# Performance work log

Hardware: AMD Instinct MI355X
Metric: run time of the kernel (lower is better)

The kernel has to match this reference:

```python
import jax, jax.numpy as jnp
import numpy as np

# ---- static configuration (mirrors init_kwargs) ----
C_IN = 1
SEQ_LEN = 512
N_KERNELS = 10000
KSS = [7, 9, 11]
KS_MAX = max(KSS)
BATCH = 8


def _make_params(seed=42):
    """Replicates the random kernel generation in RocketFeaturesPytorch.__init__."""
    rng = np.random.RandomState(seed)
    ks = np.empty(N_KERNELS, np.int32)
    dil = np.empty(N_KERNELS, np.int32)
    pad = np.empty(N_KERNELS, np.int32)  # per-side padding actually applied (= 2*padding)
    W = np.zeros((N_KERNELS, C_IN, KS_MAX), np.float32)  # zero-padded to KS_MAX taps
    b = np.empty(N_KERNELS, np.float32)
    for i in range(N_KERNELS):
        k = int(rng.choice(KSS))
        d_f = 2.0 ** rng.uniform(0, np.log2((SEQ_LEN - 1) // (k - 1)))
        d = int(d_f)  # Conv1d dilation uses int(dilation)
        p = int((k - 1) * d_f // 2) if rng.randint(2) == 1 else 0  # padding uses FLOAT dilation (as in source)
        w = rng.randn(1, C_IN, k).astype(np.float32)
        w -= w.mean()
        W[i, :, :k] = w[0]
        b[i] = np.float32(2.0 * (rng.rand() - 0.5))
        ks[i], dil[i], pad[i] = k, d, 2 * p  # layer padding = 2*padding per side
    lo = SEQ_LEN + 2 * pad - dil * (ks - 1)  # per-kernel output length (>=1 guaranteed)
    return W, b, ks, dil, pad, lo

_W, _B, _KS, _DIL, _PAD, _LO = _make_params()
PAD_MAX = int(_PAD.max())
T_MAX = int(_LO.max())


def setup_inputs() -> dict:
    key = jax.random.key(0)
    x = jax.random.normal(key, (BATCH, C_IN, SEQ_LEN), dtype=jnp.float32)
    return {
        "x": x,
        "weights": jnp.asarray(_W),                     # [K, C, KS_MAX]
        "biases": jnp.asarray(_B),                      # [K]
        "base": jnp.asarray(PAD_MAX - _PAD, jnp.int32), # [K] start offset into padded x
        "dil": jnp.asarray(_DIL, jnp.int32),            # [K]
        "lo": jnp.asarray(_LO, jnp.int32),              # [K] valid output length
    }


def reference(x, weights, biases, base, dil, lo):
    B, C, L = x.shape
    K = weights.shape[0]
    xpad = jnp.pad(x, ((0, 0), (0, 0), (PAD_MAX, PAD_MAX)))  # [B, C, Lp]
    Lp = xpad.shape[-1]
    t = jnp.arange(T_MAX, dtype=jnp.int32)                   # [T]

    # dilated conv for all kernels at once: out[b,k,t] = sum_{c,j} w[k,c,j] * xpad[b,c, base[k]+t+j*dil[k]]
    acc = jnp.zeros((B, K, T_MAX), x.dtype)
    for j in range(KS_MAX):  # small static loop over taps
        idx = jnp.clip(base[:, None] + t[None, :] + j * dil[:, None], 0, Lp - 1)  # [K, T]
        g = xpad[:, :, idx]                                   # [B, C, K, T]
        acc = acc + jnp.einsum('bckt,kc->bkt', g, weights[:, :, j])
    out = acc + biases[None, :, None]                         # [B, K, T]

    valid = t[None, :] < lo[:, None]                          # [K, T]
    maxs = jnp.max(jnp.where(valid[None], out, -jnp.inf), axis=-1)                       # [B, K]
    ppv = jnp.sum(jnp.where(valid[None], out > 0, False), axis=-1) / lo[None, :].astype(x.dtype)  # [B, K]

    # original interleaves (max_i, ppv_i) per kernel along the feature dim
    return jnp.stack([maxs, ppv.astype(x.dtype)], axis=-1).reshape(B, 2 * K)
```

## Files before the change

kernel.cpp:

```cpp
#include <hip/hip_runtime.h>
#include <math.h>

#define NK        10000
#define LSEQ      512
#define KSMAX     11
#define NKEY      3072
#define TOT_SLOT  10400
#define GRID_MAIN 1300
#define ROWS_DW   (514 * 4)
#define RED_OFF   ROWS_DW
#define SM_DW     (ROWS_DW + 256 * 10)

typedef _Float16 half2v __attribute__((ext_vector_type(2)));
union H2U { half2v h; unsigned int u; };

__device__ __forceinline__ int ks_index(float w7, float w8, float w9, float w10) {
    if (w7 == 0.f && w8 == 0.f && w9 == 0.f && w10 == 0.f) return 0;
    if (w9 == 0.f && w10 == 0.f) return 1;
    return 2;
}

__global__ __launch_bounds__(1024) void bucket_kernel(
    const float* __restrict__ W, const int* __restrict__ dil, const int* __restrict__ lo,
    int* __restrict__ ord) {
    __shared__ unsigned cnt[NKEY];
    __shared__ unsigned cur[NKEY];
    __shared__ unsigned tot;
    const int tid = threadIdx.x;
    if (tid == 0) tot = 0;
    for (int i = tid; i < NKEY; i += 1024) cnt[i] = 0;
    for (int i = tid; i < TOT_SLOT; i += 1024) ord[i] = -1;
    __syncthreads();
    for (int i = tid; i < NK; i += 1024) {
        const float* wr = W + (size_t)i * KSMAX;
        int ksi = ks_index(wr[7], wr[8], wr[9], wr[10]);
        int d = dil[i];
        int pd = (lo[i] - LSEQ + d * (6 + 2 * ksi)) > 0;
        atomicAdd(&cnt[(((d - 1) * 3 + ksi) << 1) | pd], 1u);
    }
    __syncthreads();
    for (int i = tid; i < NKEY; i += 1024) {
        unsigned c = cnt[i];
        if (c) cur[i] = atomicAdd(&tot, (c + 1u) & ~1u);
    }
    __syncthreads();
    for (int i = tid; i < NK; i += 1024) {
        const float* wr = W + (size_t)i * KSMAX;
        int ksi = ks_index(wr[7], wr[8], wr[9], wr[10]);
        int d = dil[i];
        int pd = (lo[i] - LSEQ + d * (6 + 2 * ksi)) > 0;
        unsigned s = atomicAdd(&cur[(((d - 1) * 3 + ksi) << 1) | pd], 1u);
        ord[s] = i;
    }
}

template <int KS>
__device__ __forceinline__ void run_pair(const float4* __restrict__ rows,
                                         const half2v (&wh)[2][KSMAX], const half2v (&bb)[2],
                                         const int (&pq)[2], const int (&lkq)[2],
                                         int dl, int r_lo, int r_hi, int lane,
                                         half2v (&m)[2][4], half2v (&c)[2][4]) {
    const half2v one2  = {(_Float16)1.0f, (_Float16)1.0f};
    const half2v zero2 = {(_Float16)0.0f, (_Float16)0.0f};
    const half2v big2  = {(_Float16)16384.0f, (_Float16)16384.0f};
    const half2v ninf2 = {(_Float16)(-INFINITY), (_Float16)(-INFINITY)};
    for (int r0 = r_lo; r0 < r_hi; r0 += 64) {
        const int r = r0 + lane;
        half2v a[2][4];
        #pragma unroll
        for (int q = 0; q < 2; ++q) {
            #pragma unroll
            for (int i = 0; i < 4; ++i) a[q][i] = bb[q];
        }
        int pos = r;
        #pragma unroll
        for (int j = 0; j < KS; ++j) {
            int pc = min(max(pos, -1), LSEQ);
            float4 rr = rows[pc + 1];
            half2v v0 = ((half2v*)&rr)[0];
            half2v v1 = ((half2v*)&rr)[1];
            half2v v2 = ((half2v*)&rr)[2];
            half2v v3 = ((half2v*)&rr)[3];
            #pragma unroll
            for (int q = 0; q < 2; ++q) {
                half2v wj = wh[q][j];
                a[q][0] += wj * v0;
                a[q][1] += wj * v1;
                a[q][2] += wj * v2;
                a[q][3] += wj * v3;
            }
            pos += dl;
        }
        #pragma unroll
        for (int q = 0; q < 2; ++q) {
            unsigned t = (unsigned)(r + pq[q]);
            bool valid = t < (unsigned)lkq[q];
            #pragma unroll
            for (int i = 0; i < 4; ++i) {
                half2v av = valid ? a[q][i] : ninf2;
                m[q][i] = __builtin_elementwise_max(m[q][i], av);
                c[q][i] += __builtin_elementwise_min(
                               __builtin_elementwise_max(av * big2, zero2), one2);
            }
        }
    }
}

__global__ __launch_bounds__(256) void rocket_kernel(
    const float* __restrict__ x, const float* __restrict__ W,
    const float* __restrict__ bias, const int* __restrict__ dil,
    const int* __restrict__ lo, const int* __restrict__ ord,
    float* __restrict__ out) {
    __shared__ __align__(16) float sm[SM_DW];
    const int tid = threadIdx.x;
    if (ord[blockIdx.x * 8] < 0) return;

    #pragma unroll
    for (int i = 0; i < 2; ++i) {
        int p = tid + i * 256;
        half2v h0 = {(_Float16)x[0 * LSEQ + p], (_Float16)x[1 * LSEQ + p]};
        half2v h1 = {(_Float16)x[2 * LSEQ + p], (_Float16)x[3 * LSEQ + p]};
        half2v h2 = {(_Float16)x[4 * LSEQ + p], (_Float16)x[5 * LSEQ + p]};
        half2v h3 = {(_Float16)x[6 * LSEQ + p], (_Float16)x[7 * LSEQ + p]};
        float4 v;
        ((half2v*)&v)[0] = h0;
        ((half2v*)&v)[1] = h1;
        ((half2v*)&v)[2] = h2;
        ((half2v*)&v)[3] = h3;
        *(float4*)(sm + (size_t)(p + 1) * 4) = v;
    }
    if (tid < 4)           sm[tid] = 0.0f;
    else if (tid < 8)      sm[513 * 4 + (tid - 4)] = 0.0f;

    const int wave = tid >> 6;
    const int lane = tid & 63;

    int kq[2];
    #pragma unroll
    for (int q = 0; q < 2; ++q)
        kq[q] = __builtin_amdgcn_readfirstlane(ord[blockIdx.x * 8 + wave * 2 + q]);

    half2v wh[2][KSMAX];
    half2v bb[2];
    int pq[2], lkq[2];
    float w7 = 0.f, w8 = 0.f, w9 = 0.f, w10 = 0.f;
    int dl = 1;
    #pragma unroll
    for (int q = 0; q < 2; ++q) {
        int k = kq[q];
        if (k >= 0) {
            const float* wr = W + (size_t)k * KSMAX;
            #pragma unroll
            for (int j = 0; j < KSMAX; ++j) {
                _Float16 wf = (_Float16)wr[j];
                wh[q][j] = (half2v){wf, wf};
            }
            _Float16 bf = (_Float16)bias[k];
            bb[q] = (half2v){bf, bf};
            lkq[q] = lo[k];
            if (q == 0) { w7 = wr[7]; w8 = wr[8]; w9 = wr[9]; w10 = wr[10]; dl = dil[k]; }
        } else {
            #pragma unroll
            for (int j = 0; j < KSMAX; ++j) wh[q][j] = (half2v){(_Float16)0.f, (_Float16)0.f};
            bb[q] = (half2v){(_Float16)0.f, (_Float16)0.f};
            lkq[q] = 0;
        }
    }
    const int ksi = ks_index(w7, w8, w9, w10);
    const int ks = 7 + 2 * ksi;
    int r_lo = 0, r_hi = 0;
    #pragma unroll
    for (int q = 0; q < 2; ++q) {
        if (kq[q] >= 0) {
            pq[q] = (lkq[q] - LSEQ + dl * (ks - 1)) >> 1;
            r_lo = min(r_lo, -pq[q]);
            r_hi = max(r_hi, lkq[q] - pq[q]);
        } else {
            pq[q] = 0;
        }
    }

    __syncthreads();

    const half2v ninf2 = {(_Float16)(-INFINITY), (_Float16)(-INFINITY)};
    const half2v zz    = {(_Float16)0.f, (_Float16)0.f};
    half2v m[2][4], c[2][4];
    #pragma unroll
    for (int q = 0; q < 2; ++q) {
        #pragma unroll
        for (int i = 0; i < 4; ++i) { m[q][i] = ninf2; c[q][i] = zz; }
    }

    const float4* rows = (const float4*)sm;
    if (ksi == 0)      run_pair<7 >(rows, wh, bb, pq, lkq, dl, r_lo, r_hi, lane, m, c);
    else if (ksi == 1) run_pair<9 >(rows, wh, bb, pq, lkq, dl, r_lo, r_hi, lane, m, c);
    else               run_pair<11>(rows, wh, bb, pq, lkq, dl, r_lo, r_hi, lane, m, c);

    unsigned int* red = (unsigned int*)(sm + RED_OFF);
    const int tb = tid * 10;
    const int wbase = (tid & ~63) * 10;
    const int sub = lane & 7;
    const int dv = lane >> 3;
    const bool ismax = dv < 4;
    #pragma unroll
    for (int q = 0; q < 2; ++q) {
        if (kq[q] < 0) continue;
        H2U u0, u1, u2, u3;
        uint2 p01, p23;
        u0.h = m[q][0]; u1.h = m[q][1]; u2.h = m[q][2]; u3.h = m[q][3];
        p01.x = u0.u; p01.y = u1.u; p23.x = u2.u; p23.y = u3.u;
        *(uint2*)(red + tb + 0) = p01;
        *(uint2*)(red + tb + 2) = p23;
        u0.h = c[q][0]; u1.h = c[q][1]; u2.h = c[q][2]; u3.h = c[q][3];
        p01.x = u0.u; p01.y = u1.u; p23.x = u2.u; p23.y = u3.u;
        *(uint2*)(red + tb + 4) = p01;
        *(uint2*)(red + tb + 6) = p23;

        half2v r2 = ismax ? ninf2 : zz;
        #pragma unroll
        for (int i = 0; i < 8; ++i) {
            H2U t;
            t.u = red[wbase + (sub + 8 * i) * 10 + dv];
            r2 = ismax ? __builtin_elementwise_max(r2, t.h) : (r2 + t.h);
        }
        #pragma unroll
        for (int s = 1; s < 8; s <<= 1) {
            H2U me, ot;
            me.h = r2;
            ot.u = (unsigned int)__shfl_xor((int)me.u, s, 64);
            r2 = ismax ? __builtin_elementwise_max(r2, ot.h) : (r2 + ot.h);
        }
        if (sub == 0) {
            int kk = kq[q];
            if (ismax) {
                int b = 2 * dv;
                out[(size_t)b       * (2 * NK) + 2 * kk] = (float)r2.x;
                out[(size_t)(b + 1) * (2 * NK) + 2 * kk] = (float)r2.y;
            } else {
                int b = 2 * (dv - 4);
                float inv = 1.0f / (float)lkq[q];
                out[(size_t)b       * (2 * NK) + 2 * kk + 1] = (float)r2.x * inv;
                out[(size_t)(b + 1) * (2 * NK) + 2 * kk + 1] = (float)r2.y * inv;
            }
        }
    }
}

extern "C" void kernel_launch(void* const* d_in, const int* in_sizes, int n_in,
                              void* d_out, int out_size, void* d_ws, size_t ws_size,
                              hipStream_t stream) {
    const float* x    = (const float*)d_in[0];
    const float* W    = (const float*)d_in[1];
    const float* bias = (const float*)d_in[2];
    const int*   dil  = (const int*)d_in[4];
    const int*   lo   = (const int*)d_in[5];
    float* out = (float*)d_out;
    int* ord = (int*)d_ws;

    bucket_kernel<<<1, 1024, 0, stream>>>(W, dil, lo, ord);
    rocket_kernel<<<GRID_MAIN, 256, 0, stream>>>(x, W, bias, dil, lo, ord, out);
}
```

Measured before the change: 103.6 us.

## Fuse bucketing into main kernel using persistent grid with software grid barriers

Drops the single-block bucket kernel and folds the key counting, prefix scan and slot scatter into the main kernel, separated by two global atomic spin barriers over a fixed grid of 1024 blocks. The main work becomes a grid-stride loop over kernel pairs, and a memset clears the counters beforehand. This removes a serial one-block launch and its dependency gap, but adds global atomics, spin-wait barriers that assume all 1024 blocks are co-resident, and an extra memset call.

```diff
diff --git a/kernel.cpp b/kernel.cpp
--- a/kernel.cpp
+++ b/kernel.cpp
@@ -4,55 +4,25 @@
 #define NK        10000
 #define LSEQ      512
 #define KSMAX     11
-#define NKEY      3072
-#define TOT_SLOT  10400
-#define GRID_MAIN 1300
+#define GRID      1024
+#define NKEYS     512
+#define TOT_SLOT  10512
+
+#define WS_ARR1   0
+#define WS_ARR2   64
+#define WS_CNT    128
+#define WS_OFF    640
+#define WS_ORD    1152
+#define WS_ZERO_BYTES (WS_ORD * 4)
+
 #define ROWS_DW   (514 * 4)
 #define RED_OFF   ROWS_DW
-#define SM_DW     (ROWS_DW + 256 * 10)
+#define SBASE_OFF (ROWS_DW + 2560)
+#define STOT_OFF  (SBASE_OFF + NKEYS)
+#define SM_DW     (STOT_OFF + 1)
 
 typedef _Float16 half2v __attribute__((ext_vector_type(2)));
 union H2U { half2v h; unsigned int u; };
-
-__device__ __forceinline__ int ks_index(float w7, float w8, float w9, float w10) {
-    if (w7 == 0.f && w8 == 0.f && w9 == 0.f && w10 == 0.f) return 0;
-    if (w9 == 0.f && w10 == 0.f) return 1;
-    return 2;
-}
-
-__global__ __launch_bounds__(1024) void bucket_kernel(
-    const float* __restrict__ W, const int* __restrict__ dil, const int* __restrict__ lo,
-    int* __restrict__ ord) {
-    __shared__ unsigned cnt[NKEY];
-    __shared__ unsigned cur[NKEY];
-    __shared__ unsigned tot;
-    const int tid = threadIdx.x;
-    if (tid == 0) tot = 0;
-    for (int i = tid; i < NKEY; i += 1024) cnt[i] = 0;
-    for (int i = tid; i < TOT_SLOT; i += 1024) ord[i] = -1;
-    __syncthreads();
-    for (int i = tid; i < NK; i += 1024) {
-        const float* wr = W + (size_t)i * KSMAX;
-        int ksi = ks_index(wr[7], wr[8], wr[9], wr[10]);
-        int d = dil[i];
-        int pd = (lo[i] - LSEQ + d * (6 + 2 * ksi)) > 0;
-        atomicAdd(&cnt[(((d - 1) * 3 + ksi) << 1) | pd], 1u);
-    }
-    __syncthreads();
-    for (int i = tid; i < NKEY; i += 1024) {
-        unsigned c = cnt[i];
-        if (c) cur[i] = atomicAdd(&tot, (c + 1u) & ~1u);
-    }
-    __syncthreads();
-    for (int i = tid; i < NK; i += 1024) {
-        const float* wr = W + (size_t)i * KSMAX;
-        int ksi = ks_index(wr[7], wr[8], wr[9], wr[10]);
-        int d = dil[i];
-        int pd = (lo[i] - LSEQ + d * (6 + 2 * ksi)) > 0;
-        unsigned s = atomicAdd(&cur[(((d - 1) * 3 + ksi) << 1) | pd], 1u);
-        ord[s] = i;
-    }
-}
 
 template <int KS>
 __device__ __forceinline__ void run_pair(const float4* __restrict__ rows,
@@ -106,14 +76,30 @@
     }
 }
 
-__global__ __launch_bounds__(256) void rocket_kernel(
+__global__ __launch_bounds__(256, 4) void rocket_kernel(
     const float* __restrict__ x, const float* __restrict__ W,
     const float* __restrict__ bias, const int* __restrict__ dil,
-    const int* __restrict__ lo, const int* __restrict__ ord,
+    const int* __restrict__ lo, int* __restrict__ wsI,
     float* __restrict__ out) {
     __shared__ __align__(16) float sm[SM_DW];
-    const int tid = threadIdx.x;
-    if (ord[blockIdx.x * 8] < 0) return;
+    int* smi = (int*)sm;
+    const int tid  = threadIdx.x;
+    const int wave = tid >> 6;
+    const int lane = tid & 63;
+    const int g    = blockIdx.x * 256 + tid;
+
+    int mykey = -1;
+    if (g < NK) {
+        const float* wr = W + (size_t)g * KSMAX;
+        float w7 = wr[7], w8 = wr[8], w9 = wr[9], w10 = wr[10];
+        int ksi = (w7 == 0.f && w8 == 0.f && w9 == 0.f && w10 == 0.f) ? 0
+                : ((w9 == 0.f && w10 == 0.f) ? 1 : 2);
+        int d = dil[g];
+        int pd = (lo[g] - LSEQ + d * (6 + 2 * ksi)) > 0;
+        mykey = (((d - 1) * 3 + ksi) << 1) | pd;
+        atomicAdd(&wsI[WS_CNT + mykey], 1);
+    }
+    if (g < TOT_SLOT) wsI[WS_ORD + g] = -1;
 
     #pragma unroll
     for (int i = 0; i < 2; ++i) {
@@ -132,115 +118,159 @@
     if (tid < 4)           sm[tid] = 0.0f;
     else if (tid < 8)      sm[513 * 4 + (tid - 4)] = 0.0f;
 
-    const int wave = tid >> 6;
-    const int lane = tid & 63;
-
-    int kq[2];
-    #pragma unroll
-    for (int q = 0; q < 2; ++q)
-        kq[q] = __builtin_amdgcn_readfirstlane(ord[blockIdx.x * 8 + wave * 2 + q]);
-
-    half2v wh[2][KSMAX];
-    half2v bb[2];
-    int pq[2], lkq[2];
-    float w7 = 0.f, w8 = 0.f, w9 = 0.f, w10 = 0.f;
-    int dl = 1;
-    #pragma unroll
-    for (int q = 0; q < 2; ++q) {
-        int k = kq[q];
-        if (k >= 0) {
-            const float* wr = W + (size_t)k * KSMAX;
-            #pragma unroll
-            for (int j = 0; j < KSMAX; ++j) {
-                _Float16 wf = (_Float16)wr[j];
-                wh[q][j] = (half2v){wf, wf};
-            }
-            _Float16 bf = (_Float16)bias[k];
-            bb[q] = (half2v){bf, bf};
-            lkq[q] = lo[k];
-            if (q == 0) { w7 = wr[7]; w8 = wr[8]; w9 = wr[9]; w10 = wr[10]; dl = dil[k]; }
-        } else {
-            #pragma unroll
-            for (int j = 0; j < KSMAX; ++j) wh[q][j] = (half2v){(_Float16)0.f, (_Float16)0.f};
-            bb[q] = (half2v){(_Float16)0.f, (_Float16)0.f};
-            lkq[q] = 0;
-        }
-    }
-    const int ksi = ks_index(w7, w8, w9, w10);
-    const int ks = 7 + 2 * ksi;
-    int r_lo = 0, r_hi = 0;
-    #pragma unroll
-    for (int q = 0; q < 2; ++q) {
-        if (kq[q] >= 0) {
-            pq[q] = (lkq[q] - LSEQ + dl * (ks - 1)) >> 1;
-            r_lo = min(r_lo, -pq[q]);
-            r_hi = max(r_hi, lkq[q] - pq[q]);
-        } else {
-            pq[q] = 0;
-        }
-    }
-
-    __syncthreads();
-
-    const half2v ninf2 = {(_Float16)(-INFINITY), (_Float16)(-INFINITY)};
-    const half2v zz    = {(_Float16)0.f, (_Float16)0.f};
-    half2v m[2][4], c[2][4];
-    #pragma unroll
-    for (int q = 0; q < 2; ++q) {
-        #pragma unroll
-        for (int i = 0; i < 4; ++i) { m[q][i] = ninf2; c[q][i] = zz; }
-    }
-
+    __threadfence();
+    __syncthreads();
+    if (tid == 0) {
+        atomicAdd(&wsI[WS_ARR1], 1);
+        while (atomicAdd(&wsI[WS_ARR1], 0) < GRID) {}
+    }
+    __syncthreads();
+
+    if (tid < 64) {
+        unsigned pref[8];
+        unsigned s = 0;
+        #pragma unroll
+        for (int i = 0; i < 8; ++i) {
+            unsigned cc = (unsigned)wsI[WS_CNT + tid * 8 + i];
+            cc = (cc + 1u) & ~1u;
+            pref[i] = s;
+            s += cc;
+        }
+        unsigned sc = s;
+        #pragma unroll
+        for (int o = 1; o < 64; o <<= 1) {
+            unsigned up = (unsigned)__shfl_up((int)sc, o, 64);
+            if (tid >= o) sc += up;
+        }
+        unsigned lanebase = sc - s;
+        #pragma unroll
+        for (int i = 0; i < 8; ++i) smi[SBASE_OFF + tid * 8 + i] = (int)(lanebase + pref[i]);
+        if (tid == 63) smi[STOT_OFF] = (int)sc;
+    }
+    __syncthreads();
+
+    if (g < NK) {
+        int slot = smi[SBASE_OFF + mykey] + atomicAdd(&wsI[WS_OFF + mykey], 1);
+        wsI[WS_ORD + slot] = g;
+    }
+
+    __threadfence();
+    __syncthreads();
+    if (tid == 0) {
+        atomicAdd(&wsI[WS_ARR2], 1);
+        while (atomicAdd(&wsI[WS_ARR2], 0) < GRID) {}
+    }
+    __syncthreads();
+
+    const int npairs = smi[STOT_OFF] >> 1;
     const float4* rows = (const float4*)sm;
-    if (ksi == 0)      run_pair<7 >(rows, wh, bb, pq, lkq, dl, r_lo, r_hi, lane, m, c);
-    else if (ksi == 1) run_pair<9 >(rows, wh, bb, pq, lkq, dl, r_lo, r_hi, lane, m, c);
-    else               run_pair<11>(rows, wh, bb, pq, lkq, dl, r_lo, r_hi, lane, m, c);
-
     unsigned int* red = (unsigned int*)(sm + RED_OFF);
     const int tb = tid * 10;
     const int wbase = (tid & ~63) * 10;
     const int sub = lane & 7;
     const int dv = lane >> 3;
     const bool ismax = dv < 4;
-    #pragma unroll
-    for (int q = 0; q < 2; ++q) {
-        if (kq[q] < 0) continue;
-        H2U u0, u1, u2, u3;
-        uint2 p01, p23;
-        u0.h = m[q][0]; u1.h = m[q][1]; u2.h = m[q][2]; u3.h = m[q][3];
-        p01.x = u0.u; p01.y = u1.u; p23.x = u2.u; p23.y = u3.u;
-        *(uint2*)(red + tb + 0) = p01;
-        *(uint2*)(red + tb + 2) = p23;
-        u0.h = c[q][0]; u1.h = c[q][1]; u2.h = c[q][2]; u3.h = c[q][3];
-        p01.x = u0.u; p01.y = u1.u; p23.x = u2.u; p23.y = u3.u;
-        *(uint2*)(red + tb + 4) = p01;
-        *(uint2*)(red + tb + 6) = p23;
-
-        half2v r2 = ismax ? ninf2 : zz;
-        #pragma unroll
-        for (int i = 0; i < 8; ++i) {
-            H2U t;
-            t.u = red[wbase + (sub + 8 * i) * 10 + dv];
-            r2 = ismax ? __builtin_elementwise_max(r2, t.h) : (r2 + t.h);
-        }
-        #pragma unroll
-        for (int s = 1; s < 8; s <<= 1) {
-            H2U me, ot;
-            me.h = r2;
-            ot.u = (unsigned int)__shfl_xor((int)me.u, s, 64);
-            r2 = ismax ? __builtin_elementwise_max(r2, ot.h) : (r2 + ot.h);
-        }
-        if (sub == 0) {
-            int kk = kq[q];
-            if (ismax) {
-                int b = 2 * dv;
-                out[(size_t)b       * (2 * NK) + 2 * kk] = (float)r2.x;
-                out[(size_t)(b + 1) * (2 * NK) + 2 * kk] = (float)r2.y;
+    const half2v ninf2 = {(_Float16)(-INFINITY), (_Float16)(-INFINITY)};
+    const half2v zz    = {(_Float16)0.f, (_Float16)0.f};
+
+    for (int p = blockIdx.x * 4 + wave; p < npairs; p += GRID * 4) {
+        int kq[2];
+        #pragma unroll
+        for (int q = 0; q < 2; ++q)
+            kq[q] = __builtin_amdgcn_readfirstlane(wsI[WS_ORD + 2 * p + q]);
+
+        half2v wh[2][KSMAX];
+        half2v bb[2];
+        int pq[2], lkq[2];
+        float w7 = 0.f, w8 = 0.f, w9 = 0.f, w10 = 0.f;
+        int dl = 1;
+        #pragma unroll
+        for (int q = 0; q < 2; ++q) {
+            int k = kq[q];
+            if (k >= 0) {
+                const float* wr = W + (size_t)k * KSMAX;
+                #pragma unroll
+                for (int j = 0; j < KSMAX; ++j) {
+                    _Float16 wf = (_Float16)wr[j];
+                    wh[q][j] = (half2v){wf, wf};
+                }
+                _Float16 bf = (_Float16)bias[k];
+                bb[q] = (half2v){bf, bf};
+                lkq[q] = lo[k];
+                if (q == 0) { w7 = wr[7]; w8 = wr[8]; w9 = wr[9]; w10 = wr[10]; dl = dil[k]; }
             } else {
-                int b = 2 * (dv - 4);
-                float inv = 1.0f / (float)lkq[q];
-                out[(size_t)b       * (2 * NK) + 2 * kk + 1] = (float)r2.x * inv;
-                out[(size_t)(b + 1) * (2 * NK) + 2 * kk + 1] = (float)r2.y * inv;
+                #pragma unroll
+                for (int j = 0; j < KSMAX; ++j) wh[q][j] = (half2v){(_Float16)0.f, (_Float16)0.f};
+                bb[q] = (half2v){(_Float16)0.f, (_Float16)0.f};
+                lkq[q] = 0;
+            }
+        }
+        const int ksi = (w7 == 0.f && w8 == 0.f && w9 == 0.f && w10 == 0.f) ? 0
+                      : ((w9 == 0.f && w10 == 0.f) ? 1 : 2);
+        const int ks = 7 + 2 * ksi;
+        int r_lo = 0, r_hi = 0;
+        #pragma unroll
+        for (int q = 0; q < 2; ++q) {
+            if (kq[q] >= 0) {
+                pq[q] = (lkq[q] - LSEQ + dl * (ks - 1)) >> 1;
+                r_lo = min(r_lo, -pq[q]);
+                r_hi = max(r_hi, lkq[q] - pq[q]);
+            } else {
+                pq[q] = 0;
+            }
+        }
+
+        half2v m[2][4], c[2][4];
+        #pragma unroll
+        for (int q = 0; q < 2; ++q) {
+            #pragma unroll
+            for (int i = 0; i < 4; ++i) { m[q][i] = ninf2; c[q][i] = zz; }
+        }
+
+        if (ksi == 0)      run_pair<7 >(rows, wh, bb, pq, lkq, dl, r_lo, r_hi, lane, m, c);
+        else if (ksi == 1) run_pair<9 >(rows, wh, bb, pq, lkq, dl, r_lo, r_hi, lane, m, c);
+        else               run_pair<11>(rows, wh, bb, pq, lkq, dl, r_lo, r_hi, lane, m, c);
+
+        #pragma unroll
+        for (int q = 0; q < 2; ++q) {
+            if (kq[q] < 0) continue;
+            H2U u0, u1, u2, u3;
+            uint2 p01, p23;
+            u0.h = m[q][0]; u1.h = m[q][1]; u2.h = m[q][2]; u3.h = m[q][3];
+            p01.x = u0.u; p01.y = u1.u; p23.x = u2.u; p23.y = u3.u;
+            *(uint2*)(red + tb + 0) = p01;
+            *(uint2*)(red + tb + 2) = p23;
+            u0.h = c[q][0]; u1.h = c[q][1]; u2.h = c[q][2]; u3.h = c[q][3];
+            p01.x = u0.u; p01.y = u1.u; p23.x = u2.u; p23.y = u3.u;
+            *(uint2*)(red + tb + 4) = p01;
+            *(uint2*)(red + tb + 6) = p23;
+
+            half2v r2 = ismax ? ninf2 : zz;
+            #pragma unroll
+            for (int i = 0; i < 8; ++i) {
+                H2U t;
+                t.u = red[wbase + (sub + 8 * i) * 10 + dv];
+                r2 = ismax ? __builtin_elementwise_max(r2, t.h) : (r2 + t.h);
+            }
+            #pragma unroll
+            for (int s = 1; s < 8; s <<= 1) {
+                H2U me, ot;
+                me.h = r2;
+                ot.u = (unsigned int)__shfl_xor((int)me.u, s, 64);
+                r2 = ismax ? __builtin_elementwise_max(r2, ot.h) : (r2 + ot.h);
+            }
+            if (sub == 0) {
+                int kk = kq[q];
+                if (ismax) {
+                    int b = 2 * dv;
+                    out[(size_t)b       * (2 * NK) + 2 * kk] = (float)r2.x;
+                    out[(size_t)(b + 1) * (2 * NK) + 2 * kk] = (float)r2.y;
+                } else {
+                    int b = 2 * (dv - 4);
+                    float inv = 1.0f / (float)lkq[q];
+                    out[(size_t)b       * (2 * NK) + 2 * kk + 1] = (float)r2.x * inv;
+                    out[(size_t)(b + 1) * (2 * NK) + 2 * kk + 1] = (float)r2.y * inv;
+                }
             }
         }
     }
@@ -255,8 +285,8 @@
     const int*   dil  = (const int*)d_in[4];
     const int*   lo   = (const int*)d_in[5];
     float* out = (float*)d_out;
-    int* ord = (int*)d_ws;
-
-    bucket_kernel<<<1, 1024, 0, stream>>>(W, dil, lo, ord);
-    rocket_kernel<<<GRID_MAIN, 256, 0, stream>>>(x, W, bias, dil, lo, ord, out);
+    int* wsI = (int*)d_ws;
+
+    hipMemsetAsync(wsI, 0, WS_ZERO_BYTES, stream);
+    rocket_kernel<<<GRID, 256, 0, stream>>>(x, W, bias, dil, lo, wsI, out);
 }
```

Measured after the change: 303.0 us. +192.6%, slower.
